# Optimization experiments

Measured on AMD Instinct MI355X. Metric: run time of the kernel, lower is better.

Reference implementation:

```python
import jax, jax.numpy as jnp
import numpy as np

CLS_W = 1.0
REG_W = 1.0
POS_THR = 0.6
THR_LOW = 0.3
THR_HIGH = 0.6
N_POS = 16
N_NEG = 48
BATCH = 4096
NUM_ANCHOR = 5
FS = 17
SEARCH = 255


def make_anchors():
    # SiamRPN-style anchors: 5 aspect ratios, base size 64, stride 8, 17x17 grid
    ratios = np.array([0.33, 0.5, 1.0, 2.0, 3.0], dtype=np.float64)
    size, stride = 64.0, 8
    ws = np.sqrt(size * size / ratios)            # (K,)
    hs = ws * ratios                              # (K,)
    c = (np.arange(FS) - FS // 2) * stride + SEARCH // 2  # grid centers
    cx = np.broadcast_to(c[None, None, :], (NUM_ANCHOR, FS, FS))
    cy = np.broadcast_to(c[None, :, None], (NUM_ANCHOR, FS, FS))
    w = np.broadcast_to(ws[:, None, None], (NUM_ANCHOR, FS, FS))
    h = np.broadcast_to(hs[:, None, None], (NUM_ANCHOR, FS, FS))
    center = np.stack([cx, cy, w, h], 0).reshape(4, -1).T               # (A,4) cx,cy,w,h
    corner = np.stack([cx - w / 2, cy - h / 2, cx + w / 2, cy + h / 2], 0).reshape(4, -1).T
    return center.astype(np.float32), corner.astype(np.float32)


def setup_inputs() -> dict:
    key = jax.random.key(0)
    k1, k2, k3, k4 = jax.random.split(key, 4)
    pred_cls = jax.random.normal(k1, (BATCH, NUM_ANCHOR, FS, FS), dtype=jnp.float32)
    pred_reg = jax.random.normal(k2, (BATCH, 4, NUM_ANCHOR, FS, FS), dtype=jnp.float32)
    # valid GT boxes inside the search region, overlapping anchor sizes
    cxy = jax.random.uniform(k3, (BATCH, 2), minval=90.0, maxval=165.0)
    wh = jax.random.uniform(k4, (BATCH, 2), minval=35.0, maxval=110.0)
    gt_bbox = jnp.concatenate([cxy - wh / 2, cxy + wh / 2], axis=1).astype(jnp.float32)
    center, corner = make_anchors()
    return {
        "pred_cls": pred_cls,
        "pred_reg": pred_reg,
        "gt_bbox": gt_bbox,
        "anchor_center": jnp.asarray(center),
        "anchor_corner": jnp.asarray(corner),
    }


def jaccard(box_a, box_b):
    # box_a (N,4), box_b (A,4) in x1,y1,x2,y2 -> (N,A) IoU
    lt = jnp.maximum(box_a[:, None, :2], box_b[None, :, :2])
    rb = jnp.minimum(box_a[:, None, 2:], box_b[None, :, 2:])
    wh = jnp.clip(rb - lt, 0.0)
    inter = wh[..., 0] * wh[..., 1]
    area_a = (box_a[:, 2] - box_a[:, 0]) * (box_a[:, 3] - box_a[:, 1])
    area_b = (box_b[:, 2] - box_b[:, 0]) * (box_b[:, 3] - box_b[:, 1])
    return inter / (area_a[:, None] + area_b[None, :] - inter)


def _rand_rank(k, m, A):
    # rank of each index among masked entries under a random shuffle
    u = jax.random.uniform(k, (A,))
    s = jnp.where(m, u, jnp.inf)
    order = jnp.argsort(s)
    return jnp.zeros((A,), jnp.int32).at[order].set(jnp.arange(A, dtype=jnp.int32))


def _forward(pred_cls, pred_reg, gt_bbox, anchor_center, anchor_corner):
    N = pred_cls.shape[0]
    A = anchor_center.shape[0]
    iou = jaccard(gt_bbox, anchor_corner)                       # (N,A)
    matched = jnp.where(iou > THR_HIGH, 1.0, jnp.where(iou < THR_LOW, 0.0, -1.0))
    ks = jax.random.split(jax.random.key(42), 2 * N)
    kpos, kneg = ks[:N], ks[N:]

    def per_sample(cls, reg, gt, mask, kp, kn):
        clsf = cls.reshape(-1)                                  # (A,)
        regf = reg.reshape(4, -1).T                             # (A,4)
        pos = mask == 1.0
        neg = mask == 0.0
        n_pos = jnp.sum(pos).astype(jnp.int32)
        n_neg = jnp.sum(neg).astype(jnp.int32)
        rp = _rand_rank(kp, pos, A)
        rn = _rand_rank(kn, neg, A)
        k_p = jnp.minimum(n_pos, N_POS)                         # sampled positives
        k_n_cap = jnp.where(n_pos > 0, 3 * n_pos, N_NEG)        # int(n_pos*48/16) = 3*n_pos
        k_n = jnp.minimum(n_neg, k_n_cap)
        sel_p = pos & (rp < k_p)
        sel_n = neg & (rn < k_n)
        bce_p = jnp.logaddexp(0.0, -clsf)                       # BCEWithLogits, target 1
        bce_n = jnp.logaddexp(0.0, clsf)                        # BCEWithLogits, target 0
        denom = jnp.maximum(k_p + k_n, 1).astype(clsf.dtype)
        loss_cls_i = (jnp.sum(bce_p * sel_p) + jnp.sum(bce_n * sel_n)) / denom
        acc_i = (jnp.sum((clsf >= POS_THR) & pos) + jnp.sum((clsf < POS_THR) & (~pos))).astype(clsf.dtype) / A
        gcx = (gt[0] + gt[2]) * 0.5
        gcy = (gt[1] + gt[3]) * 0.5
        gw = gt[2] - gt[0]
        gh = gt[3] - gt[1]
        acx, acy, aw, ah = anchor_center[:, 0], anchor_center[:, 1], anchor_center[:, 2], anchor_center[:, 3]
        tgt = jnp.stack([(gcx - acx) / aw, (gcy - acy) / ah, jnp.log(gw / aw), jnp.log(gh / ah)], axis=1)
        np_safe = jnp.maximum(n_pos, 1).astype(clsf.dtype)
        loss_reg_i = jnp.where(n_pos > 0,
                               jnp.sum(((regf - tgt) ** 2) * pos[:, None]) / (4.0 * np_safe),
                               0.0)
        return loss_cls_i, loss_reg_i, acc_i

    lc, lr, ac = jax.vmap(per_sample)(pred_cls, pred_reg, gt_bbox, matched, kpos, kneg)
    loss_cls = jnp.mean(lc)
    loss_reg = jnp.mean(lr)
    acc_cls = jnp.mean(ac)
    loss_total = CLS_W * loss_cls + REG_W * loss_reg
    return loss_total, loss_cls, loss_reg, acc_cls


def reference(pred_cls, pred_reg, gt_bbox, anchor_center, anchor_corner):
    return _forward(pred_cls, pred_reg, gt_bbox, anchor_center, anchor_corner)
```

## Files before the change

kernel.cpp:

```cpp
#include <hip/hip_runtime.h>
#include <stdint.h>
#include <math.h>


#define A_TOT 1445
#define NITER 23
#define WPB 4
#define POS_MAX 64
#define CAND_MAX 128

__device__ __forceinline__ void tf2x32(uint32_t k0, uint32_t k1, uint32_t x0, uint32_t x1,
                                       uint32_t& o0, uint32_t& o1)
{
  const uint32_t k2 = k0 ^ k1 ^ 0x1BD11BDAu;
  x0 += k0; x1 += k1;
#define TFR(r) { x0 += x1; x1 = __builtin_rotateleft32(x1, (r)); x1 ^= x0; }
  TFR(13) TFR(15) TFR(26) TFR(6)
  x0 += k1; x1 += k2 + 1u;
  TFR(17) TFR(29) TFR(16) TFR(24)
  x0 += k2; x1 += k0 + 2u;
  TFR(13) TFR(15) TFR(26) TFR(6)
  x0 += k0; x1 += k1 + 3u;
  TFR(17) TFR(29) TFR(16) TFR(24)
  x0 += k1; x1 += k2 + 4u;
  TFR(13) TFR(15) TFR(26) TFR(6)
  x0 += k2; x1 += k0 + 5u;
#undef TFR
  o0 = x0; o1 = x1;
}

__device__ __forceinline__ float lae0(float x){
  return fmaxf(x, 0.0f) + __logf(1.0f + __expf(-fabsf(x)));
}

__global__ void __launch_bounds__(WPB * 64, 4) rpn_loss_kernel(
    const float* __restrict__ pred_cls, const float* __restrict__ pred_reg,
    const float* __restrict__ gt_bbox, const float* __restrict__ anchor_center,
    const float* __restrict__ anchor_corner,
    float* __restrict__ part,
    int N)
{
  __shared__ uint32_t s_hist[WPB][256];
  __shared__ uint32_t s_cand[WPB][CAND_MAX];
  __shared__ uint32_t s_pidx[WPB][POS_MAX];
  __shared__ float    s_pcls[WPB][POS_MAX];
  __shared__ uint32_t s_cnt[WPB][2];

  const int w    = threadIdx.x >> 6;
  const int lane = threadIdx.x & 63;
  const int n    = blockIdx.x * WPB + w;

  #pragma unroll
  for (int b = 0; b < 4; b++) s_hist[w][lane * 4 + b] = 0u;
  if (lane < 2) s_cnt[w][lane] = 0u;

  const float g0 = gt_bbox[4 * n + 0];
  const float g1 = gt_bbox[4 * n + 1];
  const float g2 = gt_bbox[4 * n + 2];
  const float g3 = gt_bbox[4 * n + 3];
  const float area_a = (g2 - g0) * (g3 - g1);

  uint32_t kp0, kp1, kn0, kn1;
  tf2x32(0u, 42u, 0u, (uint32_t)n,       kp0, kp1);
  tf2x32(0u, 42u, 0u, (uint32_t)(N + n), kn0, kn1);

  const float*  cls_base = pred_cls + (size_t)n * A_TOT;
  const float4* cornv = (const float4*)anchor_corner;

  uint32_t rn[NITER];
  float    cv[NITER];
  uint32_t negbits = 0u;
  float accc = 0.0f;

  #pragma unroll
  for (int t = 0; t < NITER; t++){
    int j = lane + 64 * t;
    bool valid = (j < A_TOT);
    int jc = valid ? j : (A_TOT - 1);
    float4 cr = cornv[jc];
    float c = cls_base[jc];
    cv[t] = c;
    float ltx = fmaxf(g0, cr.x), lty = fmaxf(g1, cr.y);
    float rbx = fminf(g2, cr.z), rby = fminf(g3, cr.w);
    float inter = fmaxf(rbx - ltx, 0.0f) * fmaxf(rby - lty, 0.0f);
    float area_b = (cr.z - cr.x) * (cr.w - cr.y);
    float iou = inter / (area_a + area_b - inter);
    bool pos = valid && (iou > 0.6f);
    bool neg = valid && (iou < 0.3f);
    uint32_t o0, o1;
    tf2x32(kn0, kn1, 0u, (uint32_t)j, o0, o1);
    uint32_t r = (o0 ^ o1) >> 9;
    rn[t] = r;
    if (neg){ negbits |= (1u << t); atomicAdd(&s_hist[w][r >> 15], 1u); }
    if (pos){
      uint32_t id = atomicAdd(&s_cnt[w][0], 1u);
      if (id < POS_MAX){ s_pidx[w][id] = (uint32_t)j; s_pcls[w][id] = c; }
    }
    if (valid) accc += ((c >= 0.6f) == pos) ? 1.0f : 0.0f;
  }

  const int n_pos = min((int)s_cnt[w][0], POS_MAX);
  const int k_p = min(n_pos, 16);

  uint32_t S0, S1, S2, S3;
  {
    int b = lane * 4;
    uint32_t v0 = s_hist[w][b], v1 = s_hist[w][b+1], v2 = s_hist[w][b+2], v3 = s_hist[w][b+3];
    S0 = v0; S1 = S0 + v1; S2 = S1 + v2; S3 = S2 + v3;
    uint32_t x = S3;
    #pragma unroll
    for (int off = 1; off < 64; off <<= 1){
      uint32_t tmp = __shfl_up(x, off, 64);
      if (lane >= off) x += tmp;
    }
    uint32_t excl = x - S3;
    S0 += excl; S1 += excl; S2 += excl; S3 += excl;
    s_hist[w][b] = S0; s_hist[w][b+1] = S1; s_hist[w][b+2] = S2; s_hist[w][b+3] = S3;
  }
  const int n_neg = (int)__shfl(S3, 63, 64);
  const int k_n = min(n_neg, (n_pos > 0) ? 3 * n_pos : 48);

  int Bb = 256, m = 0;
  if (k_n > 0){
    unsigned long long bal = __ballot(S3 >= (uint32_t)k_n);
    int fl = __ffsll((unsigned long long)bal) - 1;
    uint32_t t0 = __shfl(S0, fl, 64), t1 = __shfl(S1, fl, 64), t2 = __shfl(S2, fl, 64);
    int sub = (t0 >= (uint32_t)k_n) ? 0 : ((t1 >= (uint32_t)k_n) ? 1 : ((t2 >= (uint32_t)k_n) ? 2 : 3));
    Bb = fl * 4 + sub;
    uint32_t before = (Bb == 0) ? 0u : s_hist[w][Bb - 1];
    m = k_n - (int)before;
  }

  float lc = 0.0f, lr = 0.0f;
  if (n_pos > 0){
    uint32_t myr = 0u, myj = 0u; float myc = 0.0f;
    if (lane < n_pos){
      myj = s_pidx[w][lane];
      myc = s_pcls[w][lane];
      uint32_t o0, o1;
      tf2x32(kp0, kp1, 0u, myj, o0, o1);
      myr = (o0 ^ o1) >> 9;
    }
    int rank = 0;
    for (int l = 0; l < n_pos; l++){
      uint32_t r2 = __shfl(myr, l, 64), j2 = __shfl(myj, l, 64);
      if (lane < n_pos && (r2 < myr || (r2 == myr && j2 < myj))) rank++;
    }
    if (lane < n_pos){
      if (rank < k_p) lc += lae0(-myc);
      float gcx = (g0 + g2) * 0.5f, gcy = (g1 + g3) * 0.5f;
      float gw = g2 - g0, gh = g3 - g1;
      float4 ce = ((const float4*)anchor_center)[myj];
      const float* reg_base = pred_reg + (size_t)n * 4 * A_TOT;
      float t0 = (gcx - ce.x) / ce.z;
      float t1 = (gcy - ce.y) / ce.w;
      float t2 = __logf(gw / ce.z);
      float t3 = __logf(gh / ce.w);
      float d0 = reg_base[myj]             - t0;
      float d1 = reg_base[A_TOT + myj]     - t1;
      float d2 = reg_base[2 * A_TOT + myj] - t2;
      float d3 = reg_base[3 * A_TOT + myj] - t3;
      lr = d0 * d0 + d1 * d1 + d2 * d2 + d3 * d3;
    }
  }

  if (k_n > 0){
    #pragma unroll
    for (int t = 0; t < NITER; t++){
      if (negbits & (1u << t)){
        int bin = (int)(rn[t] >> 15);
        if (bin < Bb) lc += lae0(cv[t]);
        else if (bin == Bb){
          uint32_t id = atomicAdd(&s_cnt[w][1], 1u);
          if (id < CAND_MAX)
            s_cand[w][id] = ((rn[t] & 0x7FFFu) << 11) | (uint32_t)(lane + 64 * t);
        }
      }
    }
    const int L = min((int)s_cnt[w][1], CAND_MAX);
    for (int c = lane; c < L; c += 64){
      uint32_t my = s_cand[w][c];
      int rank = 0;
      for (int l = 0; l < L; l++) rank += (s_cand[w][l] < my) ? 1 : 0;
      if (rank < m) lc += lae0(cls_base[my & 0x7FFu]);
    }
  }

  float v0 = lc, v1 = lr, v2 = accc;
  #pragma unroll
  for (int off = 32; off > 0; off >>= 1){
    v0 += __shfl_down(v0, off, 64);
    v1 += __shfl_down(v1, off, 64);
    v2 += __shfl_down(v2, off, 64);
  }
  if (lane == 0){
    int denom = k_p + k_n; if (denom < 1) denom = 1;
    part[n]         = v0 / (float)denom;
    part[N + n]     = (n_pos > 0) ? (v1 / (4.0f * (float)n_pos)) : 0.0f;
    part[2 * N + n] = v2 * (1.0f / (float)A_TOT);
  }
}

__global__ void __launch_bounds__(256) reduce_kernel(const float* __restrict__ part,
                                                     float* __restrict__ out, int N)
{
  const int tid = threadIdx.x;
  float lc = 0.0f, lr = 0.0f, ac = 0.0f;
  for (int i = tid; i < N; i += 256){
    lc += part[i];
    lr += part[N + i];
    ac += part[2 * N + i];
  }
  __shared__ float s[12];
  #pragma unroll
  for (int off = 32; off > 0; off >>= 1){
    lc += __shfl_down(lc, off, 64);
    lr += __shfl_down(lr, off, 64);
    ac += __shfl_down(ac, off, 64);
  }
  const int wave = tid >> 6, lane = tid & 63;
  if (lane == 0){ s[wave] = lc; s[4 + wave] = lr; s[8 + wave] = ac; }
  __syncthreads();
  if (tid == 0){
    float LC = s[0] + s[1] + s[2] + s[3];
    float LR = s[4] + s[5] + s[6] + s[7];
    float AC = s[8] + s[9] + s[10] + s[11];
    float inv = 1.0f / (float)N;
    LC *= inv; LR *= inv; AC *= inv;
    out[0] = LC + LR;
    out[1] = LC;
    out[2] = LR;
    out[3] = AC;
  }
}

extern "C" void kernel_launch(void* const* d_in, const int* in_sizes, int n_in,
                              void* d_out, int out_size, void* d_ws, size_t ws_size,
                              hipStream_t stream)
{
  const float* pred_cls = (const float*)d_in[0];
  const float* pred_reg = (const float*)d_in[1];
  const float* gt_bbox  = (const float*)d_in[2];
  const float* a_center = (const float*)d_in[3];
  const float* a_corner = (const float*)d_in[4];
  float* part = (float*)d_ws;
  float* out  = (float*)d_out;

  const int N = in_sizes[2] / 4;

  hipLaunchKernelGGL(rpn_loss_kernel, dim3(N / WPB), dim3(WPB * 64), 0, stream,
                     pred_cls, pred_reg, gt_bbox, a_center, a_corner, part, N);
  hipLaunchKernelGGL(reduce_kernel, dim3(1), dim3(256), 0, stream, part, out, N);
}
```

Before: 167.2 us.

## Spill per-anchor random keys to LDS and replace shared atomics with ballot compaction

```diff
diff --git a/kernel.cpp b/kernel.cpp
--- a/kernel.cpp
+++ b/kernel.cpp
@@ -33,26 +33,27 @@
   return fmaxf(x, 0.0f) + __logf(1.0f + __expf(-fabsf(x)));
 }
 
-__global__ void __launch_bounds__(WPB * 64, 4) rpn_loss_kernel(
+__global__ void __attribute__((amdgpu_waves_per_eu(4, 4)))
+__launch_bounds__(WPB * 64) rpn_loss_kernel(
     const float* __restrict__ pred_cls, const float* __restrict__ pred_reg,
     const float* __restrict__ gt_bbox, const float* __restrict__ anchor_center,
     const float* __restrict__ anchor_corner,
     float* __restrict__ part,
     int N)
 {
+  __shared__ uint32_t s_rnm[WPB][A_TOT];
   __shared__ uint32_t s_hist[WPB][256];
-  __shared__ uint32_t s_cand[WPB][CAND_MAX];
   __shared__ uint32_t s_pidx[WPB][POS_MAX];
   __shared__ float    s_pcls[WPB][POS_MAX];
-  __shared__ uint32_t s_cnt[WPB][2];
+  __shared__ uint32_t s_cand[WPB][CAND_MAX];
 
   const int w    = threadIdx.x >> 6;
   const int lane = threadIdx.x & 63;
   const int n    = blockIdx.x * WPB + w;
+  const uint64_t lmask_lt = (1ull << lane) - 1ull;
 
   #pragma unroll
   for (int b = 0; b < 4; b++) s_hist[w][lane * 4 + b] = 0u;
-  if (lane < 2) s_cnt[w][lane] = 0u;
 
   const float g0 = gt_bbox[4 * n + 0];
   const float g1 = gt_bbox[4 * n + 1];
@@ -67,9 +68,7 @@
   const float*  cls_base = pred_cls + (size_t)n * A_TOT;
   const float4* cornv = (const float4*)anchor_corner;
 
-  uint32_t rn[NITER];
-  float    cv[NITER];
-  uint32_t negbits = 0u;
+  uint32_t posCnt = 0u, negCnt = 0u;
   float accc = 0.0f;
 
   #pragma unroll
@@ -79,7 +78,6 @@
     int jc = valid ? j : (A_TOT - 1);
     float4 cr = cornv[jc];
     float c = cls_base[jc];
-    cv[t] = c;
     float ltx = fmaxf(g0, cr.x), lty = fmaxf(g1, cr.y);
     float rbx = fminf(g2, cr.z), rby = fminf(g3, cr.w);
     float inter = fmaxf(rbx - ltx, 0.0f) * fmaxf(rby - lty, 0.0f);
@@ -90,17 +88,23 @@
     uint32_t o0, o1;
     tf2x32(kn0, kn1, 0u, (uint32_t)j, o0, o1);
     uint32_t r = (o0 ^ o1) >> 9;
-    rn[t] = r;
-    if (neg){ negbits |= (1u << t); atomicAdd(&s_hist[w][r >> 15], 1u); }
+    uint32_t enc = pos ? 2u : (neg ? 0u : 1u);
+    if (valid) s_rnm[w][j] = (r << 2) | enc;
+    if (neg)   atomicAdd(&s_hist[w][r >> 15], 1u);
+    uint64_t pm = __ballot(pos);
     if (pos){
-      uint32_t id = atomicAdd(&s_cnt[w][0], 1u);
+      uint32_t id = posCnt + (uint32_t)__popcll(pm & lmask_lt);
       if (id < POS_MAX){ s_pidx[w][id] = (uint32_t)j; s_pcls[w][id] = c; }
     }
-    if (valid) accc += ((c >= 0.6f) == pos) ? 1.0f : 0.0f;
-  }
-
-  const int n_pos = min((int)s_cnt[w][0], POS_MAX);
+    posCnt += (uint32_t)__popcll(pm);
+    negCnt += (uint32_t)__popcll(__ballot(neg));
+    accc += (valid && ((c >= 0.6f) == pos)) ? 1.0f : 0.0f;
+  }
+
+  const int n_pos = min((int)posCnt, POS_MAX);
+  const int n_neg = (int)negCnt;
   const int k_p = min(n_pos, 16);
+  const int k_n = min(n_neg, (n_pos > 0) ? 3 * n_pos : 48);
 
   uint32_t S0, S1, S2, S3;
   {
@@ -117,13 +121,11 @@
     S0 += excl; S1 += excl; S2 += excl; S3 += excl;
     s_hist[w][b] = S0; s_hist[w][b+1] = S1; s_hist[w][b+2] = S2; s_hist[w][b+3] = S3;
   }
-  const int n_neg = (int)__shfl(S3, 63, 64);
-  const int k_n = min(n_neg, (n_pos > 0) ? 3 * n_pos : 48);
 
   int Bb = 256, m = 0;
   if (k_n > 0){
     unsigned long long bal = __ballot(S3 >= (uint32_t)k_n);
-    int fl = __ffsll((unsigned long long)bal) - 1;
+    int fl = __ffsll(bal) - 1;
     uint32_t t0 = __shfl(S0, fl, 64), t1 = __shfl(S1, fl, 64), t2 = __shfl(S2, fl, 64);
     int sub = (t0 >= (uint32_t)k_n) ? 0 : ((t1 >= (uint32_t)k_n) ? 1 : ((t2 >= (uint32_t)k_n) ? 2 : 3));
     Bb = fl * 4 + sub;
@@ -165,21 +167,27 @@
   }
 
   if (k_n > 0){
+    uint32_t candCnt = 0u;
     #pragma unroll
     for (int t = 0; t < NITER; t++){
-      if (negbits & (1u << t)){
-        int bin = (int)(rn[t] >> 15);
-        if (bin < Bb) lc += lae0(cv[t]);
-        else if (bin == Bb){
-          uint32_t id = atomicAdd(&s_cnt[w][1], 1u);
-          if (id < CAND_MAX)
-            s_cand[w][id] = ((rn[t] & 0x7FFFu) << 11) | (uint32_t)(lane + 64 * t);
-        }
+      int j = lane + 64 * t;
+      bool valid = (j < A_TOT);
+      uint32_t word = valid ? s_rnm[w][j] : 1u;
+      bool isneg = (word & 3u) == 0u;
+      int bin = (int)(word >> 17);
+      if (isneg && bin < Bb) lc += lae0(cls_base[j]);
+      bool inB = isneg && (bin == Bb);
+      uint64_t bm = __ballot(inB);
+      if (inB){
+        uint32_t id = candCnt + (uint32_t)__popcll(bm & lmask_lt);
+        if (id < CAND_MAX)
+          s_cand[w][id] = (((word >> 2) & 0x7FFFu) << 11) | (uint32_t)j;
       }
-    }
-    const int L = min((int)s_cnt[w][1], CAND_MAX);
-    for (int c = lane; c < L; c += 64){
-      uint32_t my = s_cand[w][c];
+      candCnt += (uint32_t)__popcll(bm);
+    }
+    const int L = min((int)candCnt, CAND_MAX);
+    for (int c2 = lane; c2 < L; c2 += 64){
+      uint32_t my = s_cand[w][c2];
       int rank = 0;
       for (int l = 0; l < L; l++) rank += (s_cand[w][l] < my) ? 1 : 0;
       if (rank < m) lc += lae0(cls_base[my & 0x7FFu]);
```

After: 172.0 us. 2.8% more time.
